# Optimization experiments

Hardware: AMD Instinct MI355X
Metric: run time of the kernel (lower is better)

Reference implementation:

```python
import jax, jax.numpy as jnp
import numpy as np

B, S, DIM = 2, 2048, 1536
H = 12            # n_heads (SIGMA)
HD = DIM // H     # head_dim = 128
SIGMA = 12        # anchors per query: 6 local + 4 strided + 2 global
STRIDE_STEP = 5   # SOPFR


def setup_inputs() -> dict:
    key = jax.random.key(0)
    k0, k1, k2 = jax.random.split(key, 3)
    s = 0.02
    return {
        "x": jax.random.normal(k0, (B, S, DIM), dtype=jnp.float32),
        "Wqkv": jax.random.normal(k1, (DIM, 3 * DIM), dtype=jnp.float32) * s,
        "bqkv": jnp.zeros((3 * DIM,), dtype=jnp.float32),
        "Wout": jax.random.normal(k2, (DIM, DIM), dtype=jnp.float32) * s,
        "bout": jnp.zeros((DIM,), dtype=jnp.float32),
        # Egyptian-fraction init: [W_LOCAL, W_STRIDE, W_GLOBAL] = [1/2, 1/3, 1/6]
        "group_scale": jnp.array([0.5, 1.0 / 3.0, 1.0 / 6.0], dtype=jnp.float32),
    }


def _anchor_indices(seq_len):
    # (S, 12) int32: 6 local offsets, 4 strided offsets, then global {0, S-1}
    pos = jnp.arange(seq_len, dtype=jnp.int32)
    offs = jnp.array([-3, -2, -1, 1, 2, 3,
                      -2 * STRIDE_STEP, -STRIDE_STEP, STRIDE_STEP, 2 * STRIDE_STEP],
                     dtype=jnp.int32)
    a = jnp.clip(pos[:, None] + offs[None, :], 0, seq_len - 1)
    glob = jnp.stack([jnp.zeros_like(pos), jnp.full_like(pos, seq_len - 1)], axis=1)
    return jnp.concatenate([a, glob], axis=1)


def reference(x, Wqkv, bqkv, Wout, bout, group_scale):
    b, s, d_model = x.shape
    # QKV projection -> (3, B, H, S, HD)
    qkv = (x @ Wqkv + bqkv).reshape(b, s, 3, H, HD).transpose(2, 0, 3, 1, 4)
    q, k, v = qkv[0], qkv[1], qkv[2]
    scale = HD ** -0.5

    anchor = _anchor_indices(s)                 # (S, SIGMA)
    k_anchors = jnp.take(k, anchor, axis=2)     # (B, H, S, SIGMA, HD)
    v_anchors = jnp.take(v, anchor, axis=2)     # (B, H, S, SIGMA, HD)

    attn = jnp.einsum('bhsd,bhsad->bhsa', q, k_anchors) * scale

    gw = jax.nn.softmax(group_scale)            # (3,)
    weight_per_anchor = jnp.concatenate([
        jnp.broadcast_to(gw[0], (6,)),   # local
        jnp.broadcast_to(gw[1], (4,)),   # strided
        jnp.broadcast_to(gw[2], (2,)),   # global
    ])                                          # (SIGMA,)
    attn = attn + jnp.log(weight_per_anchor)    # broadcast over (B,H,S,·)

    attn = jax.nn.softmax(attn, axis=-1)
    attn = jnp.nan_to_num(attn, nan=0.0)

    out = jnp.einsum('bhsa,bhsad->bhsd', attn, v_anchors)
    out = out.transpose(0, 2, 1, 3).reshape(b, s, d_model)
    return out @ Wout + bout
```

## Files before the change

kernel.cpp:

```cpp
#include <hip/hip_runtime.h>
#include <hip/hip_bf16.h>
#include <cstdint>
#include <math.h>

#define B_    2
#define S_    2048
#define DIM_  1536
#define H_    12
#define HD_   128
#define TRI_  4608
#define M_    4096

typedef __attribute__((ext_vector_type(8)))  __bf16 bf16x8;
typedef __attribute__((ext_vector_type(4)))  __bf16 bf16x4;
typedef __attribute__((ext_vector_type(4)))  float  floatx4;
typedef __attribute__((ext_vector_type(16))) float  floatx16;

typedef __attribute__((address_space(3))) uint8_t       lds_u8;
typedef const __attribute__((address_space(1))) uint8_t glob_u8;

__global__ __launch_bounds__(256) void prep(const float* __restrict__ W1,
                                            __bf16* __restrict__ O1,
                                            const float* __restrict__ W2,
                                            __bf16* __restrict__ O2,
                                            const float* __restrict__ x,
                                            __bf16* __restrict__ x_bf) {
    const int T1 = (TRI_ / 64) * (DIM_ / 64);
    const int T2 = (DIM_ / 64) * (DIM_ / 64);
    int blk = blockIdx.x;
    const int t = threadIdx.x;

    if (blk >= T1 + T2) {
        blk -= T1 + T2;
        int i = blk * 256 + t;
        float4 v = ((const float4*)x)[i];
        bf16x4 o;
        o.x = (__bf16)v.x; o.y = (__bf16)v.y; o.z = (__bf16)v.z; o.w = (__bf16)v.w;
        *(bf16x4*)(x_bf + (size_t)i * 4) = o;
        return;
    }

    const float* in; __bf16* out; int R, C, c0, r0;
    if (blk < T1) {
        in = W1; out = O1; R = DIM_; C = TRI_;
        c0 = (blk % (TRI_ / 64)) * 64; r0 = (blk / (TRI_ / 64)) * 64;
    } else {
        blk -= T1;
        in = W2; out = O2; R = DIM_; C = DIM_;
        c0 = (blk % (DIM_ / 64)) * 64; r0 = (blk / (DIM_ / 64)) * 64;
    }
    __shared__ float tile[64][65];
    const int c4 = t & 15, r = t >> 4;
    #pragma unroll
    for (int i = 0; i < 64; i += 16) {
        float4 v = *(const float4*)&in[(size_t)(r0 + r + i) * C + c0 + c4 * 4];
        tile[r + i][c4 * 4 + 0] = v.x;
        tile[r + i][c4 * 4 + 1] = v.y;
        tile[r + i][c4 * 4 + 2] = v.z;
        tile[r + i][c4 * 4 + 3] = v.w;
    }
    __syncthreads();
    const int cc = t >> 2, ch = t & 3;
    #pragma unroll
    for (int cho = 0; cho < 8; cho += 4) {
        int chh = ch + cho;
        bf16x8 o;
        #pragma unroll
        for (int k = 0; k < 8; ++k) o[k] = (__bf16)tile[chh * 8 + k][cc];
        *(bf16x8*)&out[(size_t)(c0 + cc) * R + r0 + chh * 8] = o;
    }
}

__global__ __launch_bounds__(256, 3) void gemm_qkv(const __bf16* __restrict__ A,
                                                   const __bf16* __restrict__ Bt,
                                                   const float*  __restrict__ bias,
                                                   __bf16* __restrict__ Cout,
                                                   int Mdim, int Ndim, int Kdim) {
    __shared__ __align__(16) __bf16 sA[128 * 64];
    __shared__ __align__(16) __bf16 sB[192 * 64];

    const int ntiles = Ndim / 192;
    const int tile_n = blockIdx.x % ntiles;
    const int tile_m = blockIdx.x / ntiles;
    const int m0 = tile_m << 7, n0 = tile_n * 192;

    const int tid  = threadIdx.x;
    const int lane = tid & 63;
    const int wave = tid >> 6;
    const int wm = (wave >> 1) * 64;
    const int wn = (wave & 1) * 96;

    floatx16 acc[2][3] = {};

    const int lr8 = lane >> 3;
    const int swz = (((lane & 7) ^ lr8) * 8);

    const int m32  = lane & 31;
    const int half = lane >> 5;
    const int lx7  = lane & 7;

    for (int k0 = 0; k0 < Kdim; k0 += 64) {
        #pragma unroll
        for (int c = 0; c < 4; ++c) {
            int r0 = wave * 32 + c * 8;
            const __bf16* ga = A + (size_t)(m0 + r0 + lr8) * Kdim + k0 + swz;
            __builtin_amdgcn_global_load_lds((glob_u8*)ga, (lds_u8*)&sA[r0 * 64], 16, 0, 0);
        }
        #pragma unroll
        for (int c = 0; c < 6; ++c) {
            int r0 = wave * 48 + c * 8;
            const __bf16* gb = Bt + (size_t)(n0 + r0 + lr8) * Kdim + k0 + swz;
            __builtin_amdgcn_global_load_lds((glob_u8*)gb, (lds_u8*)&sB[r0 * 64], 16, 0, 0);
        }
        __syncthreads();

        #pragma unroll
        for (int ks = 0; ks < 4; ++ks) {
            const int ko = (((ks * 2 + half) ^ lx7) * 8);
            bf16x8 af[2], bfr[3];
            #pragma unroll
            for (int i = 0; i < 2; ++i)
                af[i] = *(const bf16x8*)&sA[(wm + i * 32 + m32) * 64 + ko];
            #pragma unroll
            for (int j = 0; j < 3; ++j)
                bfr[j] = *(const bf16x8*)&sB[(wn + j * 32 + m32) * 64 + ko];
            #pragma unroll
            for (int i = 0; i < 2; ++i)
                #pragma unroll
                for (int j = 0; j < 3; ++j)
                    acc[i][j] = __builtin_amdgcn_mfma_f32_32x32x16_bf16(af[i], bfr[j], acc[i][j], 0, 0, 0);
        }
        __syncthreads();
    }

    #pragma unroll
    for (int j = 0; j < 3; ++j) {
        int gc = n0 + wn + j * 32 + m32;
        float bv = bias[gc];
        #pragma unroll
        for (int i = 0; i < 2; ++i) {
            #pragma unroll
            for (int r = 0; r < 16; ++r) {
                int gr = m0 + wm + i * 32 + (r & 3) + 8 * (r >> 2) + 4 * half;
                Cout[(size_t)gr * Ndim + gc] = (__bf16)(acc[i][j][r] + bv);
            }
        }
    }
}

__global__ __launch_bounds__(256, 3) void gemm_out(const __bf16* __restrict__ A,
                                                   const __bf16* __restrict__ Bt,
                                                   const float*  __restrict__ bias,
                                                   float* __restrict__ Cout,
                                                   int Mdim, int Ndim, int Kdim) {
    __shared__ __align__(16) __bf16 sA[2][64 * 64];
    __shared__ __align__(16) __bf16 sB[2][128 * 64];

    const int ntiles = Ndim >> 7;
    const int tile_n = blockIdx.x % ntiles;
    const int tile_m = blockIdx.x / ntiles;
    const int m0 = tile_m << 6, n0 = tile_n << 7;

    const int tid  = threadIdx.x;
    const int lane = tid & 63;
    const int wave = tid >> 6;
    const int wm = (wave >> 1) * 32;
    const int wn = (wave & 1) * 64;

    floatx4 acc[2][4] = {};

    const int lr8 = lane >> 3;
    const int swz = ((lane & 7) ^ lr8) * 8;

    const int row  = lane & 15;
    const int quad = lane >> 4;

    auto stage = [&](int buf, int kk) {
        #pragma unroll
        for (int c = 0; c < 2; ++c) {
            int r0 = wave * 16 + c * 8;
            const __bf16* ga = A + (size_t)(m0 + r0 + lr8) * Kdim + kk + swz;
            __builtin_amdgcn_global_load_lds((glob_u8*)ga, (lds_u8*)&sA[buf][r0 * 64], 16, 0, 0);
        }
        #pragma unroll
        for (int c = 0; c < 4; ++c) {
            int r0 = wave * 32 + c * 8;
            const __bf16* gb = Bt + (size_t)(n0 + r0 + lr8) * Kdim + kk + swz;
            __builtin_amdgcn_global_load_lds((glob_u8*)gb, (lds_u8*)&sB[buf][r0 * 64], 16, 0, 0);
        }
    };

    stage(0, 0);
    for (int k0 = 0; k0 < Kdim; k0 += 64) {
        const int cur = (k0 >> 6) & 1;
        __syncthreads();
        if (k0 + 64 < Kdim) stage(cur ^ 1, k0 + 64);

        #pragma unroll
        for (int ks = 0; ks < 2; ++ks) {
            const int ck = ((ks * 4 + quad) ^ (row & 7)) * 8;
            bf16x8 af[2], bfr[4];
            #pragma unroll
            for (int i = 0; i < 2; ++i)
                af[i]  = *(const bf16x8*)&sA[cur][(wm + i * 16 + row) * 64 + ck];
            #pragma unroll
            for (int j = 0; j < 4; ++j)
                bfr[j] = *(const bf16x8*)&sB[cur][(wn + j * 16 + row) * 64 + ck];
            #pragma unroll
            for (int i = 0; i < 2; ++i)
                #pragma unroll
                for (int j = 0; j < 4; ++j)
                    acc[i][j] = __builtin_amdgcn_mfma_f32_16x16x32_bf16(af[i], bfr[j], acc[i][j], 0, 0, 0);
        }
    }

    #pragma unroll
    for (int j = 0; j < 4; ++j) {
        int gc = n0 + wn + j * 16 + row;
        float bv = bias[gc];
        #pragma unroll
        for (int i = 0; i < 2; ++i) {
            #pragma unroll
            for (int r = 0; r < 4; ++r) {
                int gr = m0 + wm + i * 16 + quad * 4 + r;
                Cout[(size_t)gr * Ndim + gc] = acc[i][j][r] + bv;
            }
        }
    }
}

#define AROWS 86
#define ATOT  2752

__global__ __launch_bounds__(256) void anchor_attn(const __bf16* __restrict__ qkv,
                                                   const float* __restrict__ group_scale,
                                                   __bf16* __restrict__ attn_out) {
    const int sc = blockIdx.x;
    const int h  = blockIdx.y;
    const int b  = blockIdx.z;
    const int s0 = sc * 64;

    __shared__ __align__(16) __bf16 sKV[2 * AROWS * 128];

    const int tid  = threadIdx.x;
    const int wave = tid >> 6;

    #pragma unroll
    for (int base = 0; base < ATOT; base += 256) {
        int i = base + tid;
        if (i < ATOT) {
            int r  = i >> 4;
            int c  = i & 15;
            int kv = (r >= AROWS) ? 1 : 0;
            int rr = r - AROWS * kv;
            int s_row = (rr < 84) ? min(max(s0 - 10 + rr, 0), S_ - 1)
                                  : (rr == 84 ? 0 : S_ - 1);
            int cs = c ^ (rr & 7);
            const __bf16* src = qkv + (size_t)(b * S_ + s_row) * TRI_
                              + DIM_ * (1 + kv) + h * HD_ + cs * 8;
            __builtin_amdgcn_global_load_lds((glob_u8*)src,
                (lds_u8*)sKV + (size_t)(base + wave * 64) * 16, 16, 0, 0);
        }
    }

    float g0 = group_scale[0], g1 = group_scale[1], g2 = group_scale[2];
    float gm = fmaxf(g0, fmaxf(g1, g2));
    float e0 = __expf(g0 - gm), e1 = __expf(g1 - gm), e2 = __expf(g2 - gm);
    float ls = __logf(e0 + e1 + e2);
    float lw0 = g0 - gm - ls, lw1 = g1 - gm - ls, lw2 = g2 - gm - ls;

    const int s_local = tid >> 2;
    const int ds      = tid & 3;
    const int s       = s0 + s_local;

    float q[32];
    {
        const __bf16* qp = qkv + (size_t)(b * S_ + s) * TRI_ + h * HD_ + ds * 32;
        #pragma unroll
        for (int j = 0; j < 4; ++j) {
            bf16x8 qv = *(const bf16x8*)(qp + j * 8);
            #pragma unroll
            for (int k = 0; k < 8; ++k) q[j * 8 + k] = (float)qv[k];
        }
    }

    int slot[12];
    const int offs[10] = {-3, -2, -1, 1, 2, 3, -10, -5, 5, 10};
    #pragma unroll
    for (int a = 0; a < 10; ++a) slot[a] = s_local + 10 + offs[a];
    slot[10] = 84; slot[11] = 85;

    __syncthreads();

    const float scale = 0.08838834764831845f;
    float p[12];
    float mx = -1e30f;
    #pragma unroll
    for (int a = 0; a < 12; ++a) {
        const int ro = slot[a] * 128;
        const int sw = slot[a] & 7;
        float d = 0.f;
        #pragma unroll
        for (int j = 0; j < 4; ++j) {
            bf16x8 kv = *(const bf16x8*)&sKV[ro + ((ds * 4 + j) ^ sw) * 8];
            #pragma unroll
            for (int k = 0; k < 8; ++k) d += q[j * 8 + k] * (float)kv[k];
        }
        d += __shfl_xor(d, 1); d += __shfl_xor(d, 2);
        float v = d * scale + (a < 6 ? lw0 : (a < 10 ? lw1 : lw2));
        p[a] = v;
        mx = fmaxf(mx, v);
    }
    float l = 0.f;
    #pragma unroll
    for (int a = 0; a < 12; ++a) { p[a] = __expf(p[a] - mx); l += p[a]; }
    float inv = 1.0f / l;

    float o[32] = {};
    #pragma unroll
    for (int a = 0; a < 12; ++a) {
        const int ro = AROWS * 128 + slot[a] * 128;
        const int sw = slot[a] & 7;
        float pa = p[a];
        #pragma unroll
        for (int j = 0; j < 4; ++j) {
            bf16x8 vv = *(const bf16x8*)&sKV[ro + ((ds * 4 + j) ^ sw) * 8];
            #pragma unroll
            for (int k = 0; k < 8; ++k) o[j * 8 + k] += pa * (float)vv[k];
        }
    }

    __bf16* op = attn_out + (size_t)(b * S_ + s) * DIM_ + h * HD_ + ds * 32;
    #pragma unroll
    for (int j = 0; j < 4; ++j) {
        bf16x8 ov;
        #pragma unroll
        for (int k = 0; k < 8; ++k) ov[k] = (__bf16)(o[j * 8 + k] * inv);
        *(bf16x8*)(op + j * 8) = ov;
    }
}

extern "C" void kernel_launch(void* const* d_in, const int* in_sizes, int n_in,
                              void* d_out, int out_size, void* d_ws, size_t ws_size,
                              hipStream_t stream) {
    const float* x    = (const float*)d_in[0];
    const float* Wqkv = (const float*)d_in[1];
    const float* bqkv = (const float*)d_in[2];
    const float* Wout = (const float*)d_in[3];
    const float* bout = (const float*)d_in[4];
    const float* gsc  = (const float*)d_in[5];
    float* out = (float*)d_out;

    char* ws = (char*)d_ws;
    __bf16* x_bf   = (__bf16*)(ws);
    __bf16* WqkvT  = (__bf16*)(ws + 12582912);
    __bf16* WoutT  = (__bf16*)(ws + 12582912 + 14155776);
    __bf16* qkv    = (__bf16*)(ws + 12582912 + 14155776 + 4718592);
    __bf16* attn   = (__bf16*)(ws + 12582912 + 14155776 + 4718592 + 37748736);

    {
        int nblk = (TRI_ / 64) * (DIM_ / 64) + (DIM_ / 64) * (DIM_ / 64)
                 + (M_ * DIM_) / 1024;
        prep<<<nblk, 256, 0, stream>>>(Wqkv, WqkvT, Wout, WoutT, x, x_bf);
    }

    gemm_qkv<<<(M_ / 128) * (TRI_ / 192), 256, 0, stream>>>(
        x_bf, WqkvT, bqkv, qkv, M_, TRI_, DIM_);

    anchor_attn<<<dim3(32, H_, B_), 256, 0, stream>>>(qkv, gsc, attn);

    gemm_out<<<(M_ / 64) * (DIM_ / 128), 256, 0, stream>>>(
        attn, WoutT, bout, out, M_, DIM_, DIM_);
}
```

Before: 217.0 us.

## Retile output GEMM to 64x192 with 32x32 MFMA, single-buffered

```diff
diff --git a/kernel.cpp b/kernel.cpp
--- a/kernel.cpp
+++ b/kernel.cpp
@@ -148,83 +148,72 @@
     }
 }
 
-__global__ __launch_bounds__(256, 3) void gemm_out(const __bf16* __restrict__ A,
+__global__ __launch_bounds__(256, 2) void gemm_out(const __bf16* __restrict__ A,
                                                    const __bf16* __restrict__ Bt,
                                                    const float*  __restrict__ bias,
                                                    float* __restrict__ Cout,
                                                    int Mdim, int Ndim, int Kdim) {
-    __shared__ __align__(16) __bf16 sA[2][64 * 64];
-    __shared__ __align__(16) __bf16 sB[2][128 * 64];
-
-    const int ntiles = Ndim >> 7;
+    __shared__ __align__(16) __bf16 sA[64 * 64];
+    __shared__ __align__(16) __bf16 sB[192 * 64];
+
+    const int ntiles = Ndim / 192;
     const int tile_n = blockIdx.x % ntiles;
     const int tile_m = blockIdx.x / ntiles;
-    const int m0 = tile_m << 6, n0 = tile_n << 7;
+    const int m0 = tile_m << 6, n0 = tile_n * 192;
 
     const int tid  = threadIdx.x;
     const int lane = tid & 63;
     const int wave = tid >> 6;
     const int wm = (wave >> 1) * 32;
-    const int wn = (wave & 1) * 64;
-
-    floatx4 acc[2][4] = {};
+    const int wn = (wave & 1) * 96;
+
+    floatx16 acc[3] = {};
 
     const int lr8 = lane >> 3;
-    const int swz = ((lane & 7) ^ lr8) * 8;
-
-    const int row  = lane & 15;
-    const int quad = lane >> 4;
-
-    auto stage = [&](int buf, int kk) {
+    const int swz = (((lane & 7) ^ lr8) * 8);
+
+    const int m32  = lane & 31;
+    const int half = lane >> 5;
+    const int lx7  = lane & 7;
+
+    for (int k0 = 0; k0 < Kdim; k0 += 64) {
         #pragma unroll
         for (int c = 0; c < 2; ++c) {
             int r0 = wave * 16 + c * 8;
-            const __bf16* ga = A + (size_t)(m0 + r0 + lr8) * Kdim + kk + swz;
-            __builtin_amdgcn_global_load_lds((glob_u8*)ga, (lds_u8*)&sA[buf][r0 * 64], 16, 0, 0);
-        }
-        #pragma unroll
-        for (int c = 0; c < 4; ++c) {
-            int r0 = wave * 32 + c * 8;
-            const __bf16* gb = Bt + (size_t)(n0 + r0 + lr8) * Kdim + kk + swz;
-            __builtin_amdgcn_global_load_lds((glob_u8*)gb, (lds_u8*)&sB[buf][r0 * 64], 16, 0, 0);
-        }
-    };
-
-    stage(0, 0);
-    for (int k0 = 0; k0 < Kdim; k0 += 64) {
-        const int cur = (k0 >> 6) & 1;
+            const __bf16* ga = A + (size_t)(m0 + r0 + lr8) * Kdim + k0 + swz;
+            __builtin_amdgcn_global_load_lds((glob_u8*)ga, (lds_u8*)&sA[r0 * 64], 16, 0, 0);
+        }
+        #pragma unroll
+        for (int c = 0; c < 6; ++c) {
+            int r0 = wave * 48 + c * 8;
+            const __bf16* gb = Bt + (size_t)(n0 + r0 + lr8) * Kdim + k0 + swz;
+            __builtin_amdgcn_global_load_lds((glob_u8*)gb, (lds_u8*)&sB[r0 * 64], 16, 0, 0);
+        }
         __syncthreads();
-        if (k0 + 64 < Kdim) stage(cur ^ 1, k0 + 64);
-
-        #pragma unroll
-        for (int ks = 0; ks < 2; ++ks) {
-            const int ck = ((ks * 4 + quad) ^ (row & 7)) * 8;
-            bf16x8 af[2], bfr[4];
-            #pragma unroll
-            for (int i = 0; i < 2; ++i)
-                af[i]  = *(const bf16x8*)&sA[cur][(wm + i * 16 + row) * 64 + ck];
-            #pragma unroll
-            for (int j = 0; j < 4; ++j)
-                bfr[j] = *(const bf16x8*)&sB[cur][(wn + j * 16 + row) * 64 + ck];
-            #pragma unroll
-            for (int i = 0; i < 2; ++i)
-                #pragma unroll
-                for (int j = 0; j < 4; ++j)
-                    acc[i][j] = __builtin_amdgcn_mfma_f32_16x16x32_bf16(af[i], bfr[j], acc[i][j], 0, 0, 0);
-        }
-    }
-
-    #pragma unroll
-    for (int j = 0; j < 4; ++j) {
-        int gc = n0 + wn + j * 16 + row;
+
+        #pragma unroll
+        for (int ks = 0; ks < 4; ++ks) {
+            const int ko = (((ks * 2 + half) ^ lx7) * 8);
+            bf16x8 af, bfr[3];
+            af = *(const bf16x8*)&sA[(wm + m32) * 64 + ko];
+            #pragma unroll
+            for (int j = 0; j < 3; ++j)
+                bfr[j] = *(const bf16x8*)&sB[(wn + j * 32 + m32) * 64 + ko];
+            #pragma unroll
+            for (int j = 0; j < 3; ++j)
+                acc[j] = __builtin_amdgcn_mfma_f32_32x32x16_bf16(af, bfr[j], acc[j], 0, 0, 0);
+        }
+        __syncthreads();
+    }
+
+    #pragma unroll
+    for (int j = 0; j < 3; ++j) {
+        int gc = n0 + wn + j * 32 + m32;
         float bv = bias[gc];
         #pragma unroll
-        for (int i = 0; i < 2; ++i) {
-            #pragma unroll
-            for (int r = 0; r < 4; ++r) {
-                int gr = m0 + wm + i * 16 + quad * 4 + r;
-                Cout[(size_t)gr * Ndim + gc] = acc[i][j][r] + bv;
-            }
+        for (int r = 0; r < 16; ++r) {
+            int gr = m0 + wm + (r & 3) + 8 * (r >> 2) + 4 * half;
+            Cout[(size_t)gr * Ndim + gc] = acc[j][r] + bv;
         }
     }
 }
@@ -369,6 +358,6 @@
 
     anchor_attn<<<dim3(32, H_, B_), 256, 0, stream>>>(qkv, gsc, attn);
 
-    gemm_out<<<(M_ / 64) * (DIM_ / 128), 256, 0, stream>>>(
+    gemm_out<<<(M_ / 64) * (DIM_ / 192), 256, 0, stream>>>(
         attn, WoutT, bout, out, M_, DIM_, DIM_);
 }
```

Measured after the change: 218.0 us. Within noise of the previous version (+0.4%).
